# Performance work log

Measured on AMD Instinct MI355X. Metric: run time of the kernel, lower is better.

Reference implementation:

```python
import jax, jax.numpy as jnp
import numpy as np

TQ, TK, H, HEADS = 2048, 2048, 1024, 16

def setup_inputs() -> dict:
    key = jax.random.key(0)
    ks = jax.random.split(key, 11)
    s = 1.0 / np.sqrt(H).astype(np.float32)
    return {
        "Q": jax.random.normal(ks[0], (TQ, H), jnp.float32),
        "K": jax.random.normal(ks[1], (TK, H), jnp.float32),
        "V": jax.random.normal(ks[2], (TK, H), jnp.float32),
        "Wq": jax.random.normal(ks[3], (H, H), jnp.float32) * s,
        "bq": jax.random.normal(ks[4], (H,), jnp.float32) * s,
        "Wk": jax.random.normal(ks[5], (H, H), jnp.float32) * s,
        "bk": jax.random.normal(ks[6], (H,), jnp.float32) * s,
        "Wv": jax.random.normal(ks[7], (H, H), jnp.float32) * s,
        "bv": jax.random.normal(ks[8], (H,), jnp.float32) * s,
        # linear_out: nn.Linear(num_heads, 1) -> weight [num_heads], bias scalar
        "Wo": jax.random.normal(ks[9], (HEADS,), jnp.float32) / np.sqrt(HEADS).astype(np.float32),
        "bo": jax.random.normal(ks[10], (), jnp.float32) / np.sqrt(HEADS).astype(np.float32),
    }

def reference(Q, K, V, Wq, bq, Wk, bk, Wv, bv, Wo, bo):
    heads = Wo.shape[0]
    # relu(linear) projections
    Q_l = jax.nn.relu(Q @ Wq.T + bq)            # [Tq, H]
    K_l = jax.nn.relu(K @ Wk.T + bk)            # [Tk, H]
    V_l = jax.nn.relu(V @ Wv.T + bv)            # [Tk, H]
    Tq, Hd = Q_l.shape
    Tk = K_l.shape[0]
    d = Hd // heads                              # head dim
    Qh = Q_l.reshape(Tq, heads, d)               # split heads (torch split+cat over dim0)
    Kh = K_l.reshape(Tk, heads, d)
    # per-head scaled scores: [Tq, Tk, heads]
    scale = np.float32(1.0 / np.sqrt(d))
    scores = jnp.einsum('qhd,khd->qkh', Qh, Kh) * scale
    # learned linear combine over heads -> [Tq, Tk]
    logits = scores @ Wo + bo
    attn = jax.nn.softmax(logits, axis=1)        # softmax over Tk
    out = attn @ V_l                             # [Tq, H]
    return out, attn.T                           # attention.transpose(1,0) -> [Tk, Tq]
```

## Files before the change

kernel.cpp:

```cpp
#include <hip/hip_runtime.h>
#include <stdint.h>


#define TQ 2048
#define TK 2048
#define HD 1024

#define DEVI __device__ __forceinline__

typedef __attribute__((ext_vector_type(8))) short bf16x8;
typedef __attribute__((ext_vector_type(4))) float f32x4;
typedef __attribute__((ext_vector_type(4))) unsigned short u16x4;
typedef unsigned short ushort_t;

DEVI unsigned short f2bf(float f) {
  uint32_t u = __builtin_bit_cast(uint32_t, f);
  u += 0x7FFFu + ((u >> 16) & 1u);
  return (unsigned short)(u >> 16);
}
DEVI float bf2f(unsigned short h) {
  uint32_t u = ((uint32_t)h) << 16;
  return __builtin_bit_cast(float, u);
}
DEVI void gload_lds16(const void* g, void* l) {
  __builtin_amdgcn_global_load_lds((const __attribute__((address_space(1))) void*)g,
                                   (__attribute__((address_space(3))) void*)l,
                                   16, 0, 0);
}
template<int N> DEVI void wait_vm() { asm volatile("s_waitcnt vmcnt(%0)" :: "n"(N) : "memory"); }
DEVI void wait_lgkm0() { asm volatile("s_waitcnt lgkmcnt(0)" ::: "memory"); }
#define SBAR() __builtin_amdgcn_s_barrier()

template<int BN>
DEVI void stageT(const unsigned short* __restrict__ A, const unsigned short* __restrict__ B,
                 int lda, int ldb, int k0, unsigned short* buf, int tid) {
#pragma unroll
  for (int i = 0; i < 2; i++) {
    int c = i * 512 + tid;
    int r = c >> 3;
    int cs = (c & 7) ^ (r & 7);
    gload_lds16(A + (size_t)r * lda + k0 + cs * 8, buf + c * 8);
  }
#pragma unroll
  for (int i = 0; i < BN / 64; i++) {
    int c = i * 512 + tid;
    int r = c >> 3;
    int cs = (c & 7) ^ (r & 7);
    gload_lds16(B + (size_t)r * ldb + k0 + cs * 8, buf + 8192 + c * 8);
  }
}

template<int BN>
DEVI void computeT(const unsigned short* lA, const unsigned short* lB, f32x4 acc[4][2],
                   int wr, int wc, int l15, int hi) {
  constexpr int FM = (BN == 128) ? 4 : 2;
  constexpr int WMR = (BN == 128) ? 64 : 32;
#pragma unroll
  for (int kk = 0; kk < 2; kk++) {
    bf16x8 af[4], bfr[2];
#pragma unroll
    for (int f = 0; f < FM; f++) {
      int ra = wr * WMR + f * 16 + l15;
      int ca = (kk * 4 + hi) ^ (ra & 7);
      af[f] = *(const bf16x8*)(lA + ra * 64 + ca * 8);
    }
#pragma unroll
    for (int f = 0; f < 2; f++) {
      int rb = wc * 32 + f * 16 + l15;
      int cb = (kk * 4 + hi) ^ (rb & 7);
      bfr[f] = *(const bf16x8*)(lB + rb * 64 + cb * 8);
    }
#pragma unroll
    for (int fm = 0; fm < FM; fm++)
#pragma unroll
      for (int fn = 0; fn < 2; fn++)
        acc[fm][fn] = __builtin_amdgcn_mfma_f32_16x16x32_bf16(af[fm], bfr[fn], acc[fm][fn], 0, 0, 0);
  }
}

template<int BN, int NKT>
DEVI void mfma_pipeline(const unsigned short* __restrict__ A, const unsigned short* __restrict__ B,
                        int lda, int ldb, unsigned short* lds, f32x4 acc[4][2]) {
  constexpr int FM = (BN == 128) ? 4 : 2;
  constexpr int LPS = 2 + BN / 64;
  constexpr int BSTR = 8192 + BN * 64;
  const int tid = threadIdx.x;
  const int lane = tid & 63, wave = tid >> 6;
  const int l15 = lane & 15, hi = lane >> 4;
  const int wr = (BN == 128) ? (wave >> 2) : (wave >> 1);
  const int wc = (BN == 128) ? (wave & 3) : (wave & 1);

#pragma unroll
  for (int i = 0; i < FM; i++)
#pragma unroll
    for (int j = 0; j < 2; j++) acc[i][j] = (f32x4)(0.0f);

#pragma unroll
  for (int s = 0; s < 4; s++) stageT<BN>(A, B, lda, ldb, s * 64, lds + s * BSTR, tid);

#pragma unroll 1
  for (int t = 0; t < NKT; ++t) {
    if (t < NKT - 3) wait_vm<3 * LPS>();
    else if (t == NKT - 3) wait_vm<2 * LPS>();
    else if (t == NKT - 2) wait_vm<LPS>();
    else wait_vm<0>();
    SBAR();
    unsigned short* buf = lds + (t & 3) * BSTR;
    __builtin_amdgcn_s_setprio(1);
    computeT<BN>(buf, buf + 8192, acc, wr, wc, l15, hi);
    __builtin_amdgcn_s_setprio(0);
    wait_lgkm0();
    SBAR();
    if (t + 4 < NKT) stageT<BN>(A, B, lda, ldb, (t + 4) * 64, buf, tid);
  }
}

__global__ __launch_bounds__(512)
void gemm_proj(const unsigned short* __restrict__ Qb, const unsigned short* __restrict__ Kb,
               const unsigned short* __restrict__ Vb,
               const unsigned short* __restrict__ Wqb, const unsigned short* __restrict__ Wkb,
               const unsigned short* __restrict__ Wvb,
               const float* __restrict__ bq, const float* __restrict__ bk,
               const float* __restrict__ bv, const float* __restrict__ Wo,
               unsigned short* __restrict__ Ql, unsigned short* __restrict__ Ks,
               unsigned short* __restrict__ VT) {
  __shared__ __align__(16) unsigned short lds[4 * 12288];
  const int bid = blockIdx.x;
  const int x = bid & 7, j = bid >> 3;
  const int z = j >> 5;
  const int jj = j & 31;
  const int bm = (x & 3) * 4 + (jj >> 3);
  const int bn = (x >> 2) * 8 + (jj & 7);

  const unsigned short* A = (z == 0) ? Qb : (z == 1) ? Kb : Vb;
  const unsigned short* B = (z == 0) ? Wqb : (z == 1) ? Wkb : Wvb;
  const float* bias = (z == 0) ? bq : (z == 1) ? bk : bv;

  f32x4 acc[4][2];
  mfma_pipeline<64, 16>(A + (size_t)bm * 128 * HD, B + (size_t)bn * 64 * HD, HD, HD, lds, acc);

  const int tid = threadIdx.x;
  const int lane = tid & 63, wave = tid >> 6;
  const int wr = wave >> 1, wc = wave & 1;
  const int l15 = lane & 15, hi = lane >> 4;
  const int row0 = bm * 128 + wr * 32;
  const int col0 = bn * 64 + wc * 32;

#pragma unroll
  for (int fm = 0; fm < 2; fm++)
#pragma unroll
    for (int fn = 0; fn < 2; fn++) {
      int cg = col0 + fn * 16 + l15;
      int rg = row0 + fm * 16 + hi * 4;
      float b = bias[cg];
      if (z == 2) {
        u16x4 o;
#pragma unroll
        for (int i = 0; i < 4; i++) o[i] = f2bf(fmaxf(acc[fm][fn][i] + b, 0.0f));
        *(u16x4*)(VT + (size_t)cg * TK + rg) = o;
      } else if (z == 1) {
        float s = 0.125f * Wo[cg >> 6];
#pragma unroll
        for (int i = 0; i < 4; i++)
          Ks[(size_t)(rg + i) * HD + cg] = f2bf(fmaxf(acc[fm][fn][i] + b, 0.0f) * s);
      } else {
#pragma unroll
        for (int i = 0; i < 4; i++)
          Ql[(size_t)(rg + i) * HD + cg] = f2bf(fmaxf(acc[fm][fn][i] + b, 0.0f));
      }
    }
}

__global__ __launch_bounds__(512)
void gemm_logits(const unsigned short* __restrict__ Ql, const unsigned short* __restrict__ Ks,
                 float* __restrict__ C) {
  __shared__ __align__(16) unsigned short lds[4 * 16384];
  const int bid = blockIdx.x;
  const int x = bid & 7, j = bid >> 3;
  const int bm = (x & 3) * 4 + (j >> 3);
  const int bn = (x >> 2) * 8 + (j & 7);

  f32x4 acc[4][2];
  mfma_pipeline<128, 16>(Ql + (size_t)bm * 128 * HD, Ks + (size_t)bn * 128 * HD, HD, HD, lds, acc);

  const int tid = threadIdx.x;
  const int lane = tid & 63, wave = tid >> 6;
  const int wr = wave >> 2, wc = wave & 3;
  const int l15 = lane & 15, hi = lane >> 4;
  const int row0 = bm * 128 + wr * 64;
  const int col0 = bn * 128 + wc * 32;
#pragma unroll
  for (int fm = 0; fm < 4; fm++)
#pragma unroll
    for (int fn = 0; fn < 2; fn++) {
      int cg = col0 + fn * 16 + l15;
      int rg = row0 + fm * 16 + hi * 4;
#pragma unroll
      for (int i = 0; i < 4; i++)
        C[(size_t)(rg + i) * TK + cg] = acc[fm][fn][i];
    }
}

__global__ __launch_bounds__(512)
void pv_and_transpose(const unsigned short* __restrict__ attnb, const unsigned short* __restrict__ VT,
                      float* __restrict__ outp, float* __restrict__ attnT) {
  __shared__ __align__(16) unsigned short lds[4 * 16384];
  const int bid = blockIdx.x;
  const int tid = threadIdx.x;
  if (bid < 128) {
    const int x = bid & 7, j = bid >> 3;
    const int bm = (x & 3) * 4 + (j >> 2);
    const int bn = (x >> 2) * 4 + (j & 3);
    f32x4 acc[4][2];
    mfma_pipeline<128, 32>(attnb + (size_t)bm * 128 * TK, VT + (size_t)bn * 128 * TK,
                           TK, TK, lds, acc);
    const int lane = tid & 63, wave = tid >> 6;
    const int wr = wave >> 2, wc = wave & 3;
    const int l15 = lane & 15, hi = lane >> 4;
    const int row0 = bm * 128 + wr * 64;
    const int col0 = bn * 128 + wc * 32;
#pragma unroll
    for (int fm = 0; fm < 4; fm++)
#pragma unroll
      for (int fn = 0; fn < 2; fn++) {
        int cg = col0 + fn * 16 + l15;
        int rg = row0 + fm * 16 + hi * 4;
#pragma unroll
        for (int i = 0; i < 4; i++)
          outp[(size_t)(rg + i) * HD + cg] = acc[fm][fn][i];
      }
  } else {
    unsigned short (*tile)[68] = reinterpret_cast<unsigned short (*)[68]>(lds);
    const int q0 = bid - 128;
    const int tr = (q0 >> 5) * 64;
    const int tc = (q0 & 31) * 64;
#pragma unroll
    for (int i = 0; i < 2; i++) {
      int q = i * 512 + tid;
      int r = q >> 4;
      int c4 = (q & 15) * 4;
      u16x4 v = *(const u16x4*)(attnb + (size_t)(tr + r) * TK + tc + c4);
      *(u16x4*)(&tile[r][c4]) = v;
    }
    __syncthreads();
#pragma unroll
    for (int i = 0; i < 2; i++) {
      int q = i * 512 + tid;
      int c = q >> 4;
      int r4 = (q & 15) * 4;
      f32x4 o;
#pragma unroll
      for (int jx = 0; jx < 4; jx++) o[jx] = bf2f(tile[r4 + jx][c]);
      *(f32x4*)(attnT + (size_t)(tc + c) * TQ + tr + r4) = o;
    }
  }
}

__global__ __launch_bounds__(256)
void softmax_k(const float* __restrict__ logits, unsigned short* __restrict__ attnb) {
  const int row = blockIdx.x;
  const int tid = threadIdx.x;
  const int lane = tid & 63;
  const int wave = tid >> 6;
  const float* lr = logits + (size_t)row * TK;

  f32x4 v0 = *(const f32x4*)(lr + tid * 8);
  f32x4 v1 = *(const f32x4*)(lr + tid * 8 + 4);
  float x[8];
#pragma unroll
  for (int j = 0; j < 4; j++) { x[j] = v0[j]; x[4 + j] = v1[j]; }

  float m = x[0];
#pragma unroll
  for (int j = 1; j < 8; j++) m = fmaxf(m, x[j]);
  for (int o = 32; o > 0; o >>= 1) m = fmaxf(m, __shfl_xor(m, o));
  __shared__ float redm[4], reds[4];
  if (lane == 0) redm[wave] = m;
  __syncthreads();
  m = fmaxf(fmaxf(redm[0], redm[1]), fmaxf(redm[2], redm[3]));

  const float L2E = 1.44269504088896341f;
  float e[8];
  float s = 0.0f;
#pragma unroll
  for (int j = 0; j < 8; j++) { e[j] = exp2f((x[j] - m) * L2E); s += e[j]; }
  for (int o = 32; o > 0; o >>= 1) s += __shfl_xor(s, o);
  if (lane == 0) reds[wave] = s;
  __syncthreads();
  s = reds[0] + reds[1] + reds[2] + reds[3];
  float inv = 1.0f / s;

  unsigned short* ar = attnb + (size_t)row * TK;
  u16x4 o0, o1;
#pragma unroll
  for (int j = 0; j < 4; j++) { o0[j] = f2bf(e[j] * inv); o1[j] = f2bf(e[4 + j] * inv); }
  *(u16x4*)(ar + tid * 8) = o0;
  *(u16x4*)(ar + tid * 8 + 4) = o1;
}

__global__ __launch_bounds__(256)
void cvt6(const float* __restrict__ Q, const float* __restrict__ K, const float* __restrict__ V,
          const float* __restrict__ Wq, const float* __restrict__ Wk, const float* __restrict__ Wv,
          unsigned short* __restrict__ Qb, unsigned short* __restrict__ Kb,
          unsigned short* __restrict__ Vb, unsigned short* __restrict__ Wqb,
          unsigned short* __restrict__ Wkb, unsigned short* __restrict__ Wvb) {
  const int y = blockIdx.y;
  const float* s;
  unsigned short* d;
  int n4;
  switch (y) {
    case 0: s = Q;  d = Qb;  n4 = TQ * HD / 4; break;
    case 1: s = K;  d = Kb;  n4 = TK * HD / 4; break;
    case 2: s = V;  d = Vb;  n4 = TK * HD / 4; break;
    case 3: s = Wq; d = Wqb; n4 = HD * HD / 4; break;
    case 4: s = Wk; d = Wkb; n4 = HD * HD / 4; break;
    default: s = Wv; d = Wvb; n4 = HD * HD / 4; break;
  }
  int i = blockIdx.x * 256 + threadIdx.x;
  if (i < n4) {
    f32x4 v = *(const f32x4*)(s + i * 4);
    u16x4 o;
#pragma unroll
    for (int j = 0; j < 4; j++) o[j] = f2bf(v[j]);
    *(u16x4*)(d + i * 4) = o;
  }
}

extern "C" void kernel_launch(void* const* d_in, const int* in_sizes, int n_in,
                              void* d_out, int out_size, void* d_ws, size_t ws_size,
                              hipStream_t stream) {
  const float* Q  = (const float*)d_in[0];
  const float* K  = (const float*)d_in[1];
  const float* V  = (const float*)d_in[2];
  const float* Wq = (const float*)d_in[3];
  const float* bq = (const float*)d_in[4];
  const float* Wk = (const float*)d_in[5];
  const float* bk = (const float*)d_in[6];
  const float* Wv = (const float*)d_in[7];
  const float* bv = (const float*)d_in[8];
  const float* Wo = (const float*)d_in[9];

  uint8_t* w = (uint8_t*)d_ws;
  unsigned short* Qb  = (unsigned short*)(w + 0);
  unsigned short* Kb  = (unsigned short*)(w + 4194304);
  unsigned short* Vb  = (unsigned short*)(w + 8388608);
  unsigned short* Wqb = (unsigned short*)(w + 12582912);
  unsigned short* Wkb = (unsigned short*)(w + 14680064);
  unsigned short* Wvb = (unsigned short*)(w + 16777216);
  unsigned short* Ql  = (unsigned short*)(w + 18874368);
  unsigned short* Ks  = (unsigned short*)(w + 23068672);
  unsigned short* VT  = (unsigned short*)(w + 27262976);
  float*          logits = (float*)(w + 31457280);
  unsigned short* attnb  = (unsigned short*)(w + 48234496);

  float* outp  = (float*)d_out;
  float* attnT = outp + (size_t)TQ * HD;

  cvt6<<<dim3(2048, 6), dim3(256), 0, stream>>>(Q, K, V, Wq, Wk, Wv, Qb, Kb, Vb, Wqb, Wkb, Wvb);

  gemm_proj<<<dim3(768), dim3(512), 0, stream>>>(Qb, Kb, Vb, Wqb, Wkb, Wvb,
                                                 bq, bk, bv, Wo, Ql, Ks, VT);

  gemm_logits<<<dim3(256), dim3(512), 0, stream>>>(Ql, Ks, logits);

  softmax_k<<<dim3(TQ), dim3(256), 0, stream>>>(logits, attnb);

  pv_and_transpose<<<dim3(1152), dim3(512), 0, stream>>>(attnb, VT, outp, attnT);
}
```

Baseline: 83.08 us.

## Fuse fp32-to-bf16 conversion into projection GEMM loads and drop cvt6 kernel

Removes the separate conversion kernel. The projection GEMM now loads fp32 Q/K/V and weights directly into registers, converts them to bf16 and writes them swizzled into LDS. A register-staged double buffer replaces the async global-to-LDS 4-stage ring. The shared mfma_pipeline also changes to prefetch 3 tiles ahead and drops the second barrier per iteration. This saves one launch and a full write and re-read of the bf16 copies, but the GEMM now reads twice the bytes, keeps more registers live, and overlaps less work through its shallower pipeline.

```diff
diff --git a/kernel.cpp b/kernel.cpp
--- a/kernel.cpp
+++ b/kernel.cpp
@@ -51,7 +51,7 @@
 }
 
 template<int BN>
-DEVI void computeT(const unsigned short* lA, const unsigned short* lB, f32x4 acc[4][2],
+DEVI void computeT(const unsigned short* lA, const unsigned short* lB, f32x4 (*acc)[2],
                    int wr, int wc, int l15, int hi) {
   constexpr int FM = (BN == 128) ? 4 : 2;
   constexpr int WMR = (BN == 128) ? 64 : 32;
@@ -80,7 +80,7 @@
 
 template<int BN, int NKT>
 DEVI void mfma_pipeline(const unsigned short* __restrict__ A, const unsigned short* __restrict__ B,
-                        int lda, int ldb, unsigned short* lds, f32x4 acc[4][2]) {
+                        int lda, int ldb, unsigned short* lds, f32x4 (*acc)[2]) {
   constexpr int FM = (BN == 128) ? 4 : 2;
   constexpr int LPS = 2 + BN / 64;
   constexpr int BSTR = 8192 + BN * 64;
@@ -96,12 +96,11 @@
     for (int j = 0; j < 2; j++) acc[i][j] = (f32x4)(0.0f);
 
 #pragma unroll
-  for (int s = 0; s < 4; s++) stageT<BN>(A, B, lda, ldb, s * 64, lds + s * BSTR, tid);
+  for (int s = 0; s < 3; s++) stageT<BN>(A, B, lda, ldb, s * 64, lds + s * BSTR, tid);
 
 #pragma unroll 1
   for (int t = 0; t < NKT; ++t) {
-    if (t < NKT - 3) wait_vm<3 * LPS>();
-    else if (t == NKT - 3) wait_vm<2 * LPS>();
+    if (t < NKT - 2) wait_vm<2 * LPS>();
     else if (t == NKT - 2) wait_vm<LPS>();
     else wait_vm<0>();
     SBAR();
@@ -110,21 +109,91 @@
     computeT<BN>(buf, buf + 8192, acc, wr, wc, l15, hi);
     __builtin_amdgcn_s_setprio(0);
     wait_lgkm0();
+    if (t + 3 < NKT) stageT<BN>(A, B, lda, ldb, (t + 3) * 64, lds + ((t + 3) & 3) * BSTR, tid);
+  }
+}
+
+DEVI void cvtw(unsigned short* dst, const f32x4& lo, const f32x4& hi) {
+  bf16x8 o;
+#pragma unroll
+  for (int j = 0; j < 4; j++) { o[j] = (short)f2bf(lo[j]); o[4 + j] = (short)f2bf(hi[j]); }
+  *(bf16x8*)dst = o;
+}
+
+#define PROJ_LOAD(k0, a0l, a0h, a1l, a1h, bl, bh)                                   \
+  {                                                                                 \
+    int c0 = tid, r0 = c0 >> 3, g0 = c0 & 7;                                        \
+    const float* p0 = Af + (size_t)r0 * HD + (k0) + g0 * 8;                         \
+    a0l = *(const f32x4*)p0; a0h = *(const f32x4*)(p0 + 4);                         \
+    int c1 = tid + 512, r1 = c1 >> 3, g1 = c1 & 7;                                  \
+    const float* p1 = Af + (size_t)r1 * HD + (k0) + g1 * 8;                         \
+    a1l = *(const f32x4*)p1; a1h = *(const f32x4*)(p1 + 4);                         \
+    int rb = tid >> 3, gb = tid & 7;                                                \
+    const float* pb = Bf + (size_t)rb * HD + (k0) + gb * 8;                         \
+    bl = *(const f32x4*)pb; bh = *(const f32x4*)(pb + 4);                           \
+  }
+
+#define PROJ_WRITE(buf, a0l, a0h, a1l, a1h, bl, bh)                                 \
+  {                                                                                 \
+    int c0 = tid, r0 = c0 >> 3, g0 = c0 & 7;                                        \
+    cvtw((buf) + r0 * 64 + ((g0 ^ (r0 & 7)) * 8), a0l, a0h);                        \
+    int c1 = tid + 512, r1 = c1 >> 3, g1 = c1 & 7;                                  \
+    cvtw((buf) + r1 * 64 + ((g1 ^ (r1 & 7)) * 8), a1l, a1h);                        \
+    int rb = tid >> 3, gb = tid & 7;                                                \
+    cvtw((buf) + 8192 + rb * 64 + ((gb ^ (rb & 7)) * 8), bl, bh);                   \
+  }
+
+DEVI void proj_pipeline(const float* __restrict__ Af, const float* __restrict__ Bf,
+                        unsigned short* lds, f32x4 (*acc)[2]) {
+  const int tid = threadIdx.x;
+  const int lane = tid & 63, wave = tid >> 6;
+  const int l15 = lane & 15, hi = lane >> 4;
+  const int wr = wave >> 1, wc = wave & 1;
+
+#pragma unroll
+  for (int i = 0; i < 2; i++)
+#pragma unroll
+    for (int j = 0; j < 2; j++) acc[i][j] = (f32x4)(0.0f);
+
+  unsigned short* buf0 = lds;
+  unsigned short* buf1 = lds + 12288;
+
+  f32x4 Aa0l, Aa0h, Aa1l, Aa1h, Abl, Abh;
+  f32x4 Ba0l, Ba0h, Ba1l, Ba1h, Bbl, Bbh;
+  PROJ_LOAD(0, Aa0l, Aa0h, Aa1l, Aa1h, Abl, Abh);
+  PROJ_LOAD(64, Ba0l, Ba0h, Ba1l, Ba1h, Bbl, Bbh);
+
+#pragma unroll 1
+  for (int t = 0; t < 16; t += 2) {
+    wait_vm<6>();
+    PROJ_WRITE(buf0, Aa0l, Aa0h, Aa1l, Aa1h, Abl, Abh);
+    if (t + 2 < 16) PROJ_LOAD((t + 2) * 64, Aa0l, Aa0h, Aa1l, Aa1h, Abl, Abh);
+    wait_lgkm0();
     SBAR();
-    if (t + 4 < NKT) stageT<BN>(A, B, lda, ldb, (t + 4) * 64, buf, tid);
+    __builtin_amdgcn_s_setprio(1);
+    computeT<64>(buf0, buf0 + 8192, acc, wr, wc, l15, hi);
+    __builtin_amdgcn_s_setprio(0);
+    if (t == 14) wait_vm<0>(); else wait_vm<6>();
+    PROJ_WRITE(buf1, Ba0l, Ba0h, Ba1l, Ba1h, Bbl, Bbh);
+    if (t + 3 < 16) PROJ_LOAD((t + 3) * 64, Ba0l, Ba0h, Ba1l, Ba1h, Bbl, Bbh);
+    wait_lgkm0();
+    SBAR();
+    __builtin_amdgcn_s_setprio(1);
+    computeT<64>(buf1, buf1 + 8192, acc, wr, wc, l15, hi);
+    __builtin_amdgcn_s_setprio(0);
   }
 }
 
 __global__ __launch_bounds__(512)
-void gemm_proj(const unsigned short* __restrict__ Qb, const unsigned short* __restrict__ Kb,
-               const unsigned short* __restrict__ Vb,
-               const unsigned short* __restrict__ Wqb, const unsigned short* __restrict__ Wkb,
-               const unsigned short* __restrict__ Wvb,
+void gemm_proj(const float* __restrict__ Qf, const float* __restrict__ Kf,
+               const float* __restrict__ Vf,
+               const float* __restrict__ Wqf, const float* __restrict__ Wkf,
+               const float* __restrict__ Wvf,
                const float* __restrict__ bq, const float* __restrict__ bk,
                const float* __restrict__ bv, const float* __restrict__ Wo,
                unsigned short* __restrict__ Ql, unsigned short* __restrict__ Ks,
                unsigned short* __restrict__ VT) {
-  __shared__ __align__(16) unsigned short lds[4 * 12288];
+  __shared__ __align__(16) unsigned short lds[2 * 12288];
   const int bid = blockIdx.x;
   const int x = bid & 7, j = bid >> 3;
   const int z = j >> 5;
@@ -132,12 +201,12 @@
   const int bm = (x & 3) * 4 + (jj >> 3);
   const int bn = (x >> 2) * 8 + (jj & 7);
 
-  const unsigned short* A = (z == 0) ? Qb : (z == 1) ? Kb : Vb;
-  const unsigned short* B = (z == 0) ? Wqb : (z == 1) ? Wkb : Wvb;
+  const float* Af = ((z == 0) ? Qf : (z == 1) ? Kf : Vf) + (size_t)bm * 128 * HD;
+  const float* Bf = ((z == 0) ? Wqf : (z == 1) ? Wkf : Wvf) + (size_t)bn * 64 * HD;
   const float* bias = (z == 0) ? bq : (z == 1) ? bk : bv;
 
-  f32x4 acc[4][2];
-  mfma_pipeline<64, 16>(A + (size_t)bm * 128 * HD, B + (size_t)bn * 64 * HD, HD, HD, lds, acc);
+  f32x4 acc[2][2];
+  proj_pipeline(Af, Bf, lds, acc);
 
   const int tid = threadIdx.x;
   const int lane = tid & 63, wave = tid >> 6;
@@ -296,34 +365,6 @@
   for (int j = 0; j < 4; j++) { o0[j] = f2bf(e[j] * inv); o1[j] = f2bf(e[4 + j] * inv); }
   *(u16x4*)(ar + tid * 8) = o0;
   *(u16x4*)(ar + tid * 8 + 4) = o1;
-}
-
-__global__ __launch_bounds__(256)
-void cvt6(const float* __restrict__ Q, const float* __restrict__ K, const float* __restrict__ V,
-          const float* __restrict__ Wq, const float* __restrict__ Wk, const float* __restrict__ Wv,
-          unsigned short* __restrict__ Qb, unsigned short* __restrict__ Kb,
-          unsigned short* __restrict__ Vb, unsigned short* __restrict__ Wqb,
-          unsigned short* __restrict__ Wkb, unsigned short* __restrict__ Wvb) {
-  const int y = blockIdx.y;
-  const float* s;
-  unsigned short* d;
-  int n4;
-  switch (y) {
-    case 0: s = Q;  d = Qb;  n4 = TQ * HD / 4; break;
-    case 1: s = K;  d = Kb;  n4 = TK * HD / 4; break;
-    case 2: s = V;  d = Vb;  n4 = TK * HD / 4; break;
-    case 3: s = Wq; d = Wqb; n4 = HD * HD / 4; break;
-    case 4: s = Wk; d = Wkb; n4 = HD * HD / 4; break;
-    default: s = Wv; d = Wvb; n4 = HD * HD / 4; break;
-  }
-  int i = blockIdx.x * 256 + threadIdx.x;
-  if (i < n4) {
-    f32x4 v = *(const f32x4*)(s + i * 4);
-    u16x4 o;
-#pragma unroll
-    for (int j = 0; j < 4; j++) o[j] = f2bf(v[j]);
-    *(u16x4*)(d + i * 4) = o;
-  }
 }
 
 extern "C" void kernel_launch(void* const* d_in, const int* in_sizes, int n_in,
@@ -341,24 +382,16 @@
   const float* Wo = (const float*)d_in[9];
 
   uint8_t* w = (uint8_t*)d_ws;
-  unsigned short* Qb  = (unsigned short*)(w + 0);
-  unsigned short* Kb  = (unsigned short*)(w + 4194304);
-  unsigned short* Vb  = (unsigned short*)(w + 8388608);
-  unsigned short* Wqb = (unsigned short*)(w + 12582912);
-  unsigned short* Wkb = (unsigned short*)(w + 14680064);
-  unsigned short* Wvb = (unsigned short*)(w + 16777216);
-  unsigned short* Ql  = (unsigned short*)(w + 18874368);
-  unsigned short* Ks  = (unsigned short*)(w + 23068672);
-  unsigned short* VT  = (unsigned short*)(w + 27262976);
-  float*          logits = (float*)(w + 31457280);
-  unsigned short* attnb  = (unsigned short*)(w + 48234496);
+  unsigned short* Ql  = (unsigned short*)(w + 0);
+  unsigned short* Ks  = (unsigned short*)(w + 4194304);
+  unsigned short* VT  = (unsigned short*)(w + 8388608);
+  float*          logits = (float*)(w + 12582912);
+  unsigned short* attnb  = (unsigned short*)(w + 29360128);
 
   float* outp  = (float*)d_out;
   float* attnT = outp + (size_t)TQ * HD;
 
-  cvt6<<<dim3(2048, 6), dim3(256), 0, stream>>>(Q, K, V, Wq, Wk, Wv, Qb, Kb, Vb, Wqb, Wkb, Wvb);
-
-  gemm_proj<<<dim3(768), dim3(512), 0, stream>>>(Qb, Kb, Vb, Wqb, Wkb, Wvb,
+  gemm_proj<<<dim3(768), dim3(512), 0, stream>>>(Q, K, V, Wq, Wk, Wv,
                                                  bq, bk, bv, Wo, Ql, Ks, VT);
 
   gemm_logits<<<dim3(256), dim3(512), 0, stream>>>(Ql, Ks, logits);
```

Measured after the change: 73.79 us. -11.2%, faster.

## Drop second barrier via 3-stage prefetch in 4 buffers; widen proj tiles to 128x128

Applied to the files above, without the earlier changes.

The MFMA pipeline now prefetches three K-tiles ahead into a four-slot LDS ring, writing into the slot that is not being read. That lets it remove the second barrier per iteration. The projection GEMM switches from 128x64 tiles to 128x128 tiles, halving its grid from 768 to 384 blocks and raising reuse per block. The cost is fewer blocks for the projection on a many-CU GPU, so some CUs may sit idle, and the shallower prefetch depth may expose more load latency.

```diff
diff --git a/kernel.cpp b/kernel.cpp
--- a/kernel.cpp
+++ b/kernel.cpp
@@ -11,7 +11,6 @@
 typedef __attribute__((ext_vector_type(8))) short bf16x8;
 typedef __attribute__((ext_vector_type(4))) float f32x4;
 typedef __attribute__((ext_vector_type(4))) unsigned short u16x4;
-typedef unsigned short ushort_t;
 
 DEVI unsigned short f2bf(float f) {
   uint32_t u = __builtin_bit_cast(uint32_t, f);
@@ -31,7 +30,6 @@
 DEVI void wait_lgkm0() { asm volatile("s_waitcnt lgkmcnt(0)" ::: "memory"); }
 #define SBAR() __builtin_amdgcn_s_barrier()
 
-template<int BN>
 DEVI void stageT(const unsigned short* __restrict__ A, const unsigned short* __restrict__ B,
                  int lda, int ldb, int k0, unsigned short* buf, int tid) {
 #pragma unroll
@@ -42,7 +40,7 @@
     gload_lds16(A + (size_t)r * lda + k0 + cs * 8, buf + c * 8);
   }
 #pragma unroll
-  for (int i = 0; i < BN / 64; i++) {
+  for (int i = 0; i < 2; i++) {
     int c = i * 512 + tid;
     int r = c >> 3;
     int cs = (c & 7) ^ (r & 7);
@@ -50,17 +48,14 @@
   }
 }
 
-template<int BN>
-DEVI void computeT(const unsigned short* lA, const unsigned short* lB, f32x4 acc[4][2],
+DEVI void computeT(const unsigned short* lA, const unsigned short* lB, f32x4 (*acc)[2],
                    int wr, int wc, int l15, int hi) {
-  constexpr int FM = (BN == 128) ? 4 : 2;
-  constexpr int WMR = (BN == 128) ? 64 : 32;
 #pragma unroll
   for (int kk = 0; kk < 2; kk++) {
     bf16x8 af[4], bfr[2];
 #pragma unroll
-    for (int f = 0; f < FM; f++) {
-      int ra = wr * WMR + f * 16 + l15;
+    for (int f = 0; f < 4; f++) {
+      int ra = wr * 64 + f * 16 + l15;
       int ca = (kk * 4 + hi) ^ (ra & 7);
       af[f] = *(const bf16x8*)(lA + ra * 64 + ca * 8);
     }
@@ -71,47 +66,43 @@
       bfr[f] = *(const bf16x8*)(lB + rb * 64 + cb * 8);
     }
 #pragma unroll
-    for (int fm = 0; fm < FM; fm++)
+    for (int fm = 0; fm < 4; fm++)
 #pragma unroll
       for (int fn = 0; fn < 2; fn++)
         acc[fm][fn] = __builtin_amdgcn_mfma_f32_16x16x32_bf16(af[fm], bfr[fn], acc[fm][fn], 0, 0, 0);
   }
 }
 
-template<int BN, int NKT>
+template<int NKT>
 DEVI void mfma_pipeline(const unsigned short* __restrict__ A, const unsigned short* __restrict__ B,
-                        int lda, int ldb, unsigned short* lds, f32x4 acc[4][2]) {
-  constexpr int FM = (BN == 128) ? 4 : 2;
-  constexpr int LPS = 2 + BN / 64;
-  constexpr int BSTR = 8192 + BN * 64;
+                        int lda, int ldb, unsigned short* lds, f32x4 (*acc)[2]) {
+  constexpr int LPS = 4;
+  constexpr int BSTR = 16384;
   const int tid = threadIdx.x;
   const int lane = tid & 63, wave = tid >> 6;
   const int l15 = lane & 15, hi = lane >> 4;
-  const int wr = (BN == 128) ? (wave >> 2) : (wave >> 1);
-  const int wc = (BN == 128) ? (wave & 3) : (wave & 1);
-
-#pragma unroll
-  for (int i = 0; i < FM; i++)
+  const int wr = wave >> 2, wc = wave & 3;
+
+#pragma unroll
+  for (int i = 0; i < 4; i++)
 #pragma unroll
     for (int j = 0; j < 2; j++) acc[i][j] = (f32x4)(0.0f);
 
 #pragma unroll
-  for (int s = 0; s < 4; s++) stageT<BN>(A, B, lda, ldb, s * 64, lds + s * BSTR, tid);
+  for (int s = 0; s < 3; s++) stageT(A, B, lda, ldb, s * 64, lds + s * BSTR, tid);
 
 #pragma unroll 1
   for (int t = 0; t < NKT; ++t) {
-    if (t < NKT - 3) wait_vm<3 * LPS>();
-    else if (t == NKT - 3) wait_vm<2 * LPS>();
+    if (t < NKT - 2) wait_vm<2 * LPS>();
     else if (t == NKT - 2) wait_vm<LPS>();
     else wait_vm<0>();
     SBAR();
     unsigned short* buf = lds + (t & 3) * BSTR;
     __builtin_amdgcn_s_setprio(1);
-    computeT<BN>(buf, buf + 8192, acc, wr, wc, l15, hi);
+    computeT(buf, buf + 8192, acc, wr, wc, l15, hi);
     __builtin_amdgcn_s_setprio(0);
     wait_lgkm0();
-    SBAR();
-    if (t + 4 < NKT) stageT<BN>(A, B, lda, ldb, (t + 4) * 64, buf, tid);
+    if (t + 3 < NKT) stageT(A, B, lda, ldb, (t + 3) * 64, lds + ((t + 3) & 3) * BSTR, tid);
   }
 }
 
@@ -124,30 +115,30 @@
                const float* __restrict__ bv, const float* __restrict__ Wo,
                unsigned short* __restrict__ Ql, unsigned short* __restrict__ Ks,
                unsigned short* __restrict__ VT) {
-  __shared__ __align__(16) unsigned short lds[4 * 12288];
+  __shared__ __align__(16) unsigned short lds[4 * 16384];
   const int bid = blockIdx.x;
   const int x = bid & 7, j = bid >> 3;
-  const int z = j >> 5;
-  const int jj = j & 31;
-  const int bm = (x & 3) * 4 + (jj >> 3);
-  const int bn = (x >> 2) * 8 + (jj & 7);
+  const int z = j >> 4;
+  const int jj = j & 15;
+  const int bm = (x & 3) * 4 + (jj >> 2);
+  const int bn = (x >> 2) * 4 + (jj & 3);
 
   const unsigned short* A = (z == 0) ? Qb : (z == 1) ? Kb : Vb;
   const unsigned short* B = (z == 0) ? Wqb : (z == 1) ? Wkb : Wvb;
   const float* bias = (z == 0) ? bq : (z == 1) ? bk : bv;
 
   f32x4 acc[4][2];
-  mfma_pipeline<64, 16>(A + (size_t)bm * 128 * HD, B + (size_t)bn * 64 * HD, HD, HD, lds, acc);
+  mfma_pipeline<16>(A + (size_t)bm * 128 * HD, B + (size_t)bn * 128 * HD, HD, HD, lds, acc);
 
   const int tid = threadIdx.x;
   const int lane = tid & 63, wave = tid >> 6;
-  const int wr = wave >> 1, wc = wave & 1;
+  const int wr = wave >> 2, wc = wave & 3;
   const int l15 = lane & 15, hi = lane >> 4;
-  const int row0 = bm * 128 + wr * 32;
-  const int col0 = bn * 64 + wc * 32;
-
-#pragma unroll
-  for (int fm = 0; fm < 2; fm++)
+  const int row0 = bm * 128 + wr * 64;
+  const int col0 = bn * 128 + wc * 32;
+
+#pragma unroll
+  for (int fm = 0; fm < 4; fm++)
 #pragma unroll
     for (int fn = 0; fn < 2; fn++) {
       int cg = col0 + fn * 16 + l15;
@@ -181,7 +172,7 @@
   const int bn = (x >> 2) * 8 + (j & 7);
 
   f32x4 acc[4][2];
-  mfma_pipeline<128, 16>(Ql + (size_t)bm * 128 * HD, Ks + (size_t)bn * 128 * HD, HD, HD, lds, acc);
+  mfma_pipeline<16>(Ql + (size_t)bm * 128 * HD, Ks + (size_t)bn * 128 * HD, HD, HD, lds, acc);
 
   const int tid = threadIdx.x;
   const int lane = tid & 63, wave = tid >> 6;
@@ -212,8 +203,8 @@
     const int bm = (x & 3) * 4 + (j >> 2);
     const int bn = (x >> 2) * 4 + (j & 3);
     f32x4 acc[4][2];
-    mfma_pipeline<128, 32>(attnb + (size_t)bm * 128 * TK, VT + (size_t)bn * 128 * TK,
-                           TK, TK, lds, acc);
+    mfma_pipeline<32>(attnb + (size_t)bm * 128 * TK, VT + (size_t)bn * 128 * TK,
+                      TK, TK, lds, acc);
     const int lane = tid & 63, wave = tid >> 6;
     const int wr = wave >> 2, wc = wave & 3;
     const int l15 = lane & 15, hi = lane >> 4;
@@ -358,7 +349,7 @@
 
   cvt6<<<dim3(2048, 6), dim3(256), 0, stream>>>(Q, K, V, Wq, Wk, Wv, Qb, Kb, Vb, Wqb, Wkb, Wvb);
 
-  gemm_proj<<<dim3(768), dim3(512), 0, stream>>>(Qb, Kb, Vb, Wqb, Wkb, Wvb,
+  gemm_proj<<<dim3(384), dim3(512), 0, stream>>>(Qb, Kb, Vb, Wqb, Wkb, Wvb,
                                                  bq, bk, bv, Wo, Ql, Ks, VT);
 
   gemm_logits<<<dim3(256), dim3(512), 0, stream>>>(Ql, Ks, logits);
```

Result: faster. 76.32 us (-8.1%).

## Fuse all stages into one persistent kernel with grid barriers

Applied to the files above, without the earlier changes.

Replaces five kernel launches (convert, projection GEMM, logits GEMM, softmax, PV+transpose) with a single persistent 256-block kernel that separates phases with atomic-counter grid barriers. Pipeline depth drops from four to two LDS stages so the unified shared buffer fits, and the V transpose is now staged through LDS for coalesced writes. The aim is to remove launch gaps and tail effects between stages. In exchange each block does more serial work, the shallower pipeline may expose more memory latency, and correctness depends on all 256 blocks being co-resident.

```diff
diff --git a/kernel.cpp b/kernel.cpp
--- a/kernel.cpp
+++ b/kernel.cpp
@@ -5,6 +5,7 @@
 #define TQ 2048
 #define TK 2048
 #define HD 1024
+#define NB 256
 
 #define DEVI __device__ __forceinline__
 
@@ -30,6 +31,18 @@
 template<int N> DEVI void wait_vm() { asm volatile("s_waitcnt vmcnt(%0)" :: "n"(N) : "memory"); }
 DEVI void wait_lgkm0() { asm volatile("s_waitcnt lgkmcnt(0)" ::: "memory"); }
 #define SBAR() __builtin_amdgcn_s_barrier()
+
+DEVI void gridbar(int* c) {
+  __syncthreads();
+  if (threadIdx.x == 0) {
+    __threadfence();
+    atomicAdd(c, 1);
+    while (__hip_atomic_load(c, __ATOMIC_RELAXED, __HIP_MEMORY_SCOPE_AGENT) < NB)
+      __builtin_amdgcn_s_sleep(8);
+  }
+  __syncthreads();
+  __threadfence();
+}
 
 template<int BN>
 DEVI void stageT(const unsigned short* __restrict__ A, const unsigned short* __restrict__ B,
@@ -51,7 +64,7 @@
 }
 
 template<int BN>
-DEVI void computeT(const unsigned short* lA, const unsigned short* lB, f32x4 acc[4][2],
+DEVI void computeT(const unsigned short* lA, const unsigned short* lB, f32x4 (*acc)[2],
                    int wr, int wc, int l15, int hi) {
   constexpr int FM = (BN == 128) ? 4 : 2;
   constexpr int WMR = (BN == 128) ? 64 : 32;
@@ -80,7 +93,7 @@
 
 template<int BN, int NKT>
 DEVI void mfma_pipeline(const unsigned short* __restrict__ A, const unsigned short* __restrict__ B,
-                        int lda, int ldb, unsigned short* lds, f32x4 acc[4][2]) {
+                        int lda, int ldb, unsigned short* lds, f32x4 (*acc)[2]) {
   constexpr int FM = (BN == 128) ? 4 : 2;
   constexpr int LPS = 2 + BN / 64;
   constexpr int BSTR = 8192 + BN * 64;
@@ -95,118 +108,183 @@
 #pragma unroll
     for (int j = 0; j < 2; j++) acc[i][j] = (f32x4)(0.0f);
 
-#pragma unroll
-  for (int s = 0; s < 4; s++) stageT<BN>(A, B, lda, ldb, s * 64, lds + s * BSTR, tid);
+  stageT<BN>(A, B, lda, ldb, 0, lds, tid);
+  stageT<BN>(A, B, lda, ldb, 64, lds + BSTR, tid);
 
 #pragma unroll 1
   for (int t = 0; t < NKT; ++t) {
-    if (t < NKT - 3) wait_vm<3 * LPS>();
-    else if (t == NKT - 3) wait_vm<2 * LPS>();
-    else if (t == NKT - 2) wait_vm<LPS>();
+    if (t < NKT - 1) wait_vm<LPS>();
     else wait_vm<0>();
     SBAR();
-    unsigned short* buf = lds + (t & 3) * BSTR;
+    unsigned short* buf = lds + (t & 1) * BSTR;
     __builtin_amdgcn_s_setprio(1);
     computeT<BN>(buf, buf + 8192, acc, wr, wc, l15, hi);
     __builtin_amdgcn_s_setprio(0);
     wait_lgkm0();
     SBAR();
-    if (t + 4 < NKT) stageT<BN>(A, B, lda, ldb, (t + 4) * 64, buf, tid);
+    if (t + 2 < NKT) stageT<BN>(A, B, lda, ldb, (t + 2) * 64, buf, tid);
   }
 }
 
 __global__ __launch_bounds__(512)
-void gemm_proj(const unsigned short* __restrict__ Qb, const unsigned short* __restrict__ Kb,
-               const unsigned short* __restrict__ Vb,
-               const unsigned short* __restrict__ Wqb, const unsigned short* __restrict__ Wkb,
-               const unsigned short* __restrict__ Wvb,
-               const float* __restrict__ bq, const float* __restrict__ bk,
+void fused_mha(const float* __restrict__ Q, const float* __restrict__ K,
+               const float* __restrict__ V, const float* __restrict__ Wq,
+               const float* __restrict__ bq, const float* __restrict__ Wk,
+               const float* __restrict__ bk, const float* __restrict__ Wv,
                const float* __restrict__ bv, const float* __restrict__ Wo,
+               unsigned short* __restrict__ Qb, unsigned short* __restrict__ Kb,
+               unsigned short* __restrict__ Vb, unsigned short* __restrict__ Wqb,
+               unsigned short* __restrict__ Wkb, unsigned short* __restrict__ Wvb,
                unsigned short* __restrict__ Ql, unsigned short* __restrict__ Ks,
-               unsigned short* __restrict__ VT) {
-  __shared__ __align__(16) unsigned short lds[4 * 12288];
+               unsigned short* __restrict__ VT, float* __restrict__ logits,
+               unsigned short* __restrict__ attnb, float* __restrict__ outp,
+               float* __restrict__ attnT, int* __restrict__ bars) {
+  __shared__ __align__(16) unsigned short lds[32768];
   const int bid = blockIdx.x;
-  const int x = bid & 7, j = bid >> 3;
-  const int z = j >> 5;
-  const int jj = j & 31;
-  const int bm = (x & 3) * 4 + (jj >> 3);
-  const int bn = (x >> 2) * 8 + (jj & 7);
-
-  const unsigned short* A = (z == 0) ? Qb : (z == 1) ? Kb : Vb;
-  const unsigned short* B = (z == 0) ? Wqb : (z == 1) ? Wkb : Wvb;
-  const float* bias = (z == 0) ? bq : (z == 1) ? bk : bv;
-
-  f32x4 acc[4][2];
-  mfma_pipeline<64, 16>(A + (size_t)bm * 128 * HD, B + (size_t)bn * 64 * HD, HD, HD, lds, acc);
-
   const int tid = threadIdx.x;
   const int lane = tid & 63, wave = tid >> 6;
-  const int wr = wave >> 1, wc = wave & 1;
   const int l15 = lane & 15, hi = lane >> 4;
-  const int row0 = bm * 128 + wr * 32;
-  const int col0 = bn * 64 + wc * 32;
-
-#pragma unroll
-  for (int fm = 0; fm < 2; fm++)
-#pragma unroll
-    for (int fn = 0; fn < 2; fn++) {
-      int cg = col0 + fn * 16 + l15;
-      int rg = row0 + fm * 16 + hi * 4;
-      float b = bias[cg];
+
+  {
+    const float* s6[6] = {Q, K, V, Wq, Wk, Wv};
+    unsigned short* d6[6] = {Qb, Kb, Vb, Wqb, Wkb, Wvb};
+    const int n6[6] = {524288, 524288, 524288, 262144, 262144, 262144};
+#pragma unroll
+    for (int t6 = 0; t6 < 6; ++t6) {
+      const float* s = s6[t6];
+      unsigned short* d = d6[t6];
+      for (int i = bid * 512 + tid; i < n6[t6]; i += NB * 512) {
+        f32x4 v = *(const f32x4*)(s + i * 4);
+        u16x4 o;
+#pragma unroll
+        for (int j = 0; j < 4; j++) o[j] = f2bf(v[j]);
+        *(u16x4*)(d + i * 4) = o;
+      }
+    }
+  }
+  gridbar(bars + 0);
+
+  {
+    const int x = bid & 7, jj = bid >> 3;
+    const int bm = (x & 3) * 4 + (jj >> 3);
+    const int bn = (x >> 2) * 8 + (jj & 7);
+    const unsigned short* A3[3] = {Qb, Kb, Vb};
+    const unsigned short* B3[3] = {Wqb, Wkb, Wvb};
+    const float* bias3[3] = {bq, bk, bv};
+    const int wr = wave >> 1, wc = wave & 1;
+    const int row0 = bm * 128 + wr * 32;
+    const int col0 = bn * 64 + wc * 32;
+
+#pragma unroll
+    for (int z = 0; z < 3; ++z) {
+      f32x4 acc[2][2];
+      mfma_pipeline<64, 16>(A3[z] + (size_t)bm * 128 * HD, B3[z] + (size_t)bn * 64 * HD,
+                            HD, HD, lds, acc);
+      const float* bias = bias3[z];
       if (z == 2) {
-        u16x4 o;
-#pragma unroll
-        for (int i = 0; i < 4; i++) o[i] = f2bf(fmaxf(acc[fm][fn][i] + b, 0.0f));
-        *(u16x4*)(VT + (size_t)cg * TK + rg) = o;
-      } else if (z == 1) {
-        float s = 0.125f * Wo[cg >> 6];
+        unsigned short (*T)[132] = reinterpret_cast<unsigned short (*)[132]>(lds);
+#pragma unroll
+        for (int fm = 0; fm < 2; fm++)
+#pragma unroll
+          for (int fn = 0; fn < 2; fn++) {
+            int cl = wc * 32 + fn * 16 + l15;
+            float b = bias[bn * 64 + cl];
+#pragma unroll
+            for (int i = 0; i < 4; i++)
+              T[cl][wr * 32 + fm * 16 + hi * 4 + i] = f2bf(fmaxf(acc[fm][fn][i] + b, 0.0f));
+          }
+        __syncthreads();
+#pragma unroll
+        for (int i = 0; i < 4; i++) {
+          int h = i * 512 + tid;
+          int c = h >> 5;
+          int rq = h & 31;
+          u16x4 v = *(const u16x4*)(&T[c][rq * 4]);
+          *(u16x4*)(VT + (size_t)(bn * 64 + c) * TK + bm * 128 + rq * 4) = v;
+        }
+      } else {
+#pragma unroll
+        for (int fm = 0; fm < 2; fm++)
+#pragma unroll
+          for (int fn = 0; fn < 2; fn++) {
+            int cg = col0 + fn * 16 + l15;
+            int rg = row0 + fm * 16 + hi * 4;
+            float b = bias[cg];
+            if (z == 1) {
+              float s = 0.125f * Wo[cg >> 6];
+#pragma unroll
+              for (int i = 0; i < 4; i++)
+                Ks[(size_t)(rg + i) * HD + cg] = f2bf(fmaxf(acc[fm][fn][i] + b, 0.0f) * s);
+            } else {
+#pragma unroll
+              for (int i = 0; i < 4; i++)
+                Ql[(size_t)(rg + i) * HD + cg] = f2bf(fmaxf(acc[fm][fn][i] + b, 0.0f));
+            }
+          }
+      }
+      __syncthreads();
+    }
+  }
+  gridbar(bars + 1);
+
+  {
+    const int x = bid & 7, j = bid >> 3;
+    const int bm = (x & 3) * 4 + (j >> 3);
+    const int bn = (x >> 2) * 8 + (j & 7);
+    f32x4 acc[4][2];
+    mfma_pipeline<128, 16>(Ql + (size_t)bm * 128 * HD, Ks + (size_t)bn * 128 * HD,
+                           HD, HD, lds, acc);
+    const int wr = wave >> 2, wc = wave & 3;
+    const int row0 = bm * 128 + wr * 64;
+    const int col0 = bn * 128 + wc * 32;
+#pragma unroll
+    for (int fm = 0; fm < 4; fm++)
+#pragma unroll
+      for (int fn = 0; fn < 2; fn++) {
+        int cg = col0 + fn * 16 + l15;
+        int rg = row0 + fm * 16 + hi * 4;
 #pragma unroll
         for (int i = 0; i < 4; i++)
-          Ks[(size_t)(rg + i) * HD + cg] = f2bf(fmaxf(acc[fm][fn][i] + b, 0.0f) * s);
-      } else {
-#pragma unroll
-        for (int i = 0; i < 4; i++)
-          Ql[(size_t)(rg + i) * HD + cg] = f2bf(fmaxf(acc[fm][fn][i] + b, 0.0f));
-      }
-    }
-}
-
-__global__ __launch_bounds__(512)
-void gemm_logits(const unsigned short* __restrict__ Ql, const unsigned short* __restrict__ Ks,
-                 float* __restrict__ C) {
-  __shared__ __align__(16) unsigned short lds[4 * 16384];
-  const int bid = blockIdx.x;
-  const int x = bid & 7, j = bid >> 3;
-  const int bm = (x & 3) * 4 + (j >> 3);
-  const int bn = (x >> 2) * 8 + (j & 7);
-
-  f32x4 acc[4][2];
-  mfma_pipeline<128, 16>(Ql + (size_t)bm * 128 * HD, Ks + (size_t)bn * 128 * HD, HD, HD, lds, acc);
-
-  const int tid = threadIdx.x;
-  const int lane = tid & 63, wave = tid >> 6;
-  const int wr = wave >> 2, wc = wave & 3;
-  const int l15 = lane & 15, hi = lane >> 4;
-  const int row0 = bm * 128 + wr * 64;
-  const int col0 = bn * 128 + wc * 32;
-#pragma unroll
-  for (int fm = 0; fm < 4; fm++)
-#pragma unroll
-    for (int fn = 0; fn < 2; fn++) {
-      int cg = col0 + fn * 16 + l15;
-      int rg = row0 + fm * 16 + hi * 4;
-#pragma unroll
-      for (int i = 0; i < 4; i++)
-        C[(size_t)(rg + i) * TK + cg] = acc[fm][fn][i];
-    }
-}
-
-__global__ __launch_bounds__(512)
-void pv_and_transpose(const unsigned short* __restrict__ attnb, const unsigned short* __restrict__ VT,
-                      float* __restrict__ outp, float* __restrict__ attnT) {
-  __shared__ __align__(16) unsigned short lds[4 * 16384];
-  const int bid = blockIdx.x;
-  const int tid = threadIdx.x;
+          logits[(size_t)(rg + i) * TK + cg] = acc[fm][fn][i];
+      }
+  }
+  gridbar(bars + 2);
+
+  {
+    float* fred = (float*)lds;
+    const float L2E = 1.44269504088896341f;
+#pragma unroll 1
+    for (int r = 0; r < 8; ++r) {
+      const int row = bid * 8 + r;
+      const float* lr = logits + (size_t)row * TK;
+      f32x4 v = *(const f32x4*)(lr + tid * 4);
+      float m = fmaxf(fmaxf(v[0], v[1]), fmaxf(v[2], v[3]));
+#pragma unroll
+      for (int o = 32; o > 0; o >>= 1) m = fmaxf(m, __shfl_xor(m, o));
+      if (lane == 0) fred[wave] = m;
+      __syncthreads();
+      m = fred[0];
+#pragma unroll
+      for (int wv = 1; wv < 8; wv++) m = fmaxf(m, fred[wv]);
+      float e0 = exp2f((v[0] - m) * L2E), e1 = exp2f((v[1] - m) * L2E);
+      float e2 = exp2f((v[2] - m) * L2E), e3 = exp2f((v[3] - m) * L2E);
+      float s = e0 + e1 + e2 + e3;
+#pragma unroll
+      for (int o = 32; o > 0; o >>= 1) s += __shfl_xor(s, o);
+      if (lane == 0) fred[8 + wave] = s;
+      __syncthreads();
+      float st = fred[8];
+#pragma unroll
+      for (int wv = 1; wv < 8; wv++) st += fred[8 + wv];
+      float inv = 1.0f / st;
+      u16x4 o4;
+      o4[0] = f2bf(e0 * inv); o4[1] = f2bf(e1 * inv);
+      o4[2] = f2bf(e2 * inv); o4[3] = f2bf(e3 * inv);
+      *(u16x4*)(attnb + (size_t)row * TK + tid * 4) = o4;
+    }
+  }
+  gridbar(bars + 3);
+
   if (bid < 128) {
     const int x = bid & 7, j = bid >> 3;
     const int bm = (x & 3) * 4 + (j >> 2);
@@ -214,9 +292,7 @@
     f32x4 acc[4][2];
     mfma_pipeline<128, 32>(attnb + (size_t)bm * 128 * TK, VT + (size_t)bn * 128 * TK,
                            TK, TK, lds, acc);
-    const int lane = tid & 63, wave = tid >> 6;
     const int wr = wave >> 2, wc = wave & 3;
-    const int l15 = lane & 15, hi = lane >> 4;
     const int row0 = bm * 128 + wr * 64;
     const int col0 = bn * 128 + wc * 32;
 #pragma unroll
@@ -231,98 +307,32 @@
       }
   } else {
     unsigned short (*tile)[68] = reinterpret_cast<unsigned short (*)[68]>(lds);
-    const int q0 = bid - 128;
-    const int tr = (q0 >> 5) * 64;
-    const int tc = (q0 & 31) * 64;
-#pragma unroll
-    for (int i = 0; i < 2; i++) {
-      int q = i * 512 + tid;
-      int r = q >> 4;
-      int c4 = (q & 15) * 4;
-      u16x4 v = *(const u16x4*)(attnb + (size_t)(tr + r) * TK + tc + c4);
-      *(u16x4*)(&tile[r][c4]) = v;
-    }
-    __syncthreads();
-#pragma unroll
-    for (int i = 0; i < 2; i++) {
-      int q = i * 512 + tid;
-      int c = q >> 4;
-      int r4 = (q & 15) * 4;
-      f32x4 o;
-#pragma unroll
-      for (int jx = 0; jx < 4; jx++) o[jx] = bf2f(tile[r4 + jx][c]);
-      *(f32x4*)(attnT + (size_t)(tc + c) * TQ + tr + r4) = o;
-    }
-  }
-}
-
-__global__ __launch_bounds__(256)
-void softmax_k(const float* __restrict__ logits, unsigned short* __restrict__ attnb) {
-  const int row = blockIdx.x;
-  const int tid = threadIdx.x;
-  const int lane = tid & 63;
-  const int wave = tid >> 6;
-  const float* lr = logits + (size_t)row * TK;
-
-  f32x4 v0 = *(const f32x4*)(lr + tid * 8);
-  f32x4 v1 = *(const f32x4*)(lr + tid * 8 + 4);
-  float x[8];
-#pragma unroll
-  for (int j = 0; j < 4; j++) { x[j] = v0[j]; x[4 + j] = v1[j]; }
-
-  float m = x[0];
-#pragma unroll
-  for (int j = 1; j < 8; j++) m = fmaxf(m, x[j]);
-  for (int o = 32; o > 0; o >>= 1) m = fmaxf(m, __shfl_xor(m, o));
-  __shared__ float redm[4], reds[4];
-  if (lane == 0) redm[wave] = m;
-  __syncthreads();
-  m = fmaxf(fmaxf(redm[0], redm[1]), fmaxf(redm[2], redm[3]));
-
-  const float L2E = 1.44269504088896341f;
-  float e[8];
-  float s = 0.0f;
-#pragma unroll
-  for (int j = 0; j < 8; j++) { e[j] = exp2f((x[j] - m) * L2E); s += e[j]; }
-  for (int o = 32; o > 0; o >>= 1) s += __shfl_xor(s, o);
-  if (lane == 0) reds[wave] = s;
-  __syncthreads();
-  s = reds[0] + reds[1] + reds[2] + reds[3];
-  float inv = 1.0f / s;
-
-  unsigned short* ar = attnb + (size_t)row * TK;
-  u16x4 o0, o1;
-#pragma unroll
-  for (int j = 0; j < 4; j++) { o0[j] = f2bf(e[j] * inv); o1[j] = f2bf(e[4 + j] * inv); }
-  *(u16x4*)(ar + tid * 8) = o0;
-  *(u16x4*)(ar + tid * 8 + 4) = o1;
-}
-
-__global__ __launch_bounds__(256)
-void cvt6(const float* __restrict__ Q, const float* __restrict__ K, const float* __restrict__ V,
-          const float* __restrict__ Wq, const float* __restrict__ Wk, const float* __restrict__ Wv,
-          unsigned short* __restrict__ Qb, unsigned short* __restrict__ Kb,
-          unsigned short* __restrict__ Vb, unsigned short* __restrict__ Wqb,
-          unsigned short* __restrict__ Wkb, unsigned short* __restrict__ Wvb) {
-  const int y = blockIdx.y;
-  const float* s;
-  unsigned short* d;
-  int n4;
-  switch (y) {
-    case 0: s = Q;  d = Qb;  n4 = TQ * HD / 4; break;
-    case 1: s = K;  d = Kb;  n4 = TK * HD / 4; break;
-    case 2: s = V;  d = Vb;  n4 = TK * HD / 4; break;
-    case 3: s = Wq; d = Wqb; n4 = HD * HD / 4; break;
-    case 4: s = Wk; d = Wkb; n4 = HD * HD / 4; break;
-    default: s = Wv; d = Wvb; n4 = HD * HD / 4; break;
-  }
-  int i = blockIdx.x * 256 + threadIdx.x;
-  if (i < n4) {
-    f32x4 v = *(const f32x4*)(s + i * 4);
-    u16x4 o;
-#pragma unroll
-    for (int j = 0; j < 4; j++) o[j] = f2bf(v[j]);
-    *(u16x4*)(d + i * 4) = o;
+#pragma unroll 1
+    for (int it = 0; it < 8; ++it) {
+      if (it) __syncthreads();
+      const int q0 = (bid - 128) * 8 + it;
+      const int tr = (q0 >> 5) * 64;
+      const int tc = (q0 & 31) * 64;
+#pragma unroll
+      for (int i = 0; i < 2; i++) {
+        int q = i * 512 + tid;
+        int rr = q >> 4;
+        int c4 = (q & 15) * 4;
+        u16x4 v = *(const u16x4*)(attnb + (size_t)(tr + rr) * TK + tc + c4);
+        *(u16x4*)(&tile[rr][c4]) = v;
+      }
+      __syncthreads();
+#pragma unroll
+      for (int i = 0; i < 2; i++) {
+        int q = i * 512 + tid;
+        int c = q >> 4;
+        int r4 = (q & 15) * 4;
+        f32x4 o;
+#pragma unroll
+        for (int jx = 0; jx < 4; jx++) o[jx] = bf2f(tile[r4 + jx][c]);
+        *(f32x4*)(attnT + (size_t)(tc + c) * TQ + tr + r4) = o;
+      }
+    }
   }
 }
 
@@ -351,19 +361,16 @@
   unsigned short* Ks  = (unsigned short*)(w + 23068672);
   unsigned short* VT  = (unsigned short*)(w + 27262976);
   float*          logits = (float*)(w + 31457280);
-  unsigned short* attnb  = (unsigned short*)(w + 48234496);
+  unsigned short* attnb  = (unsigned short*)(w + 0);
+  int*            bars   = (int*)(w + 48234496);
 
   float* outp  = (float*)d_out;
   float* attnT = outp + (size_t)TQ * HD;
 
-  cvt6<<<dim3(2048, 6), dim3(256), 0, stream>>>(Q, K, V, Wq, Wk, Wv, Qb, Kb, Vb, Wqb, Wkb, Wvb);
-
-  gemm_proj<<<dim3(768), dim3(512), 0, stream>>>(Qb, Kb, Vb, Wqb, Wkb, Wvb,
-                                                 bq, bk, bv, Wo, Ql, Ks, VT);
-
-  gemm_logits<<<dim3(256), dim3(512), 0, stream>>>(Ql, Ks, logits);
-
-  softmax_k<<<dim3(TQ), dim3(256), 0, stream>>>(logits, attnb);
-
-  pv_and_transpose<<<dim3(1152), dim3(512), 0, stream>>>(attnb, VT, outp, attnT);
-}
+  hipMemsetAsync(bars, 0, 16, stream);
+
+  fused_mha<<<dim3(NB), dim3(512), 0, stream>>>(Q, K, V, Wq, bq, Wk, bk, Wv, bv, Wo,
+                                                Qb, Kb, Vb, Wqb, Wkb, Wvb,
+                                                Ql, Ks, VT, logits, attnb,
+                                                outp, attnT, bars);
+}
```

Measured after the change: 278.8 us. +235.5%, slower.
